# Optimization experiments

Measured on AMD Instinct MI355X. Metric: run time of the kernel, lower is better.

Reference implementation:

```python
import jax, jax.numpy as jnp
import numpy as np
from jax.scipy.linalg import solve_triangular
from jax.scipy.special import logsumexp

N, K, D = 131072, 32, 32
LOG_2PI = np.float32(np.log(2.0 * np.pi))


def setup_inputs() -> dict:
    key = jax.random.key(0)
    k1, k2, k3, k4 = jax.random.split(key, 4)
    X = jax.random.normal(k1, (N, D), dtype=jnp.float32)
    means = jax.random.normal(k2, (K, D), dtype=jnp.float32)
    chols = jax.random.normal(k3, (K, D, D), dtype=jnp.float32)
    weights = jax.random.normal(k4, (K,), dtype=jnp.float32) - 1.0  # normal_(-1, 1)
    return {"X": X, "means": means, "chols": chols, "weights": weights, "it": 0}


def _neglog_likelihood(X, means, chols, weights):
    d = X.shape[-1]
    n = X.shape[0]
    eye = jnp.eye(d, dtype=X.dtype)
    # sigmas[k] = chols[k] @ chols[k]^T + I  -> (K, D, D)
    sigmas = jnp.einsum('kij,klj->kil', chols, chols) + eye
    L = jnp.linalg.cholesky(sigmas)                      # (K, D, D)
    # per-cluster Gaussian log-densities for all points, batched
    diff = X[None, :, :] - means[:, None, :]             # (K, N, D)
    y = solve_triangular(L, diff.transpose(0, 2, 1), lower=True)  # (K, D, N)
    maha = jnp.sum(y * y, axis=1)                        # (K, N)
    logdet = 2.0 * jnp.sum(jnp.log(jnp.diagonal(L, axis1=-2, axis2=-1)), axis=-1)  # (K,)
    log_dens = -0.5 * (maha + (logdet + d * LOG_2PI)[:, None])    # (K, N)
    dens = jnp.exp(log_dens)                             # (K, N)
    # sum_{i,j} w_i w_j N_i(x) N_j(x) = (sum_k w_k N_k(x))^2
    numer = jnp.square(weights @ dens)                   # (N,)
    # pairwise normaliser Z_ij = N(mu_i; mu_j, S_i + S_j), all pairs batched
    S_ij = sigmas[:, None] + sigmas[None, :]             # (K, K, D, D)
    L_ij = jnp.linalg.cholesky(S_ij)
    dmu = means[:, None, :] - means[None, :, :]          # (K, K, D)
    y_ij = solve_triangular(L_ij, dmu[..., None], lower=True)[..., 0]  # (K, K, D)
    maha_ij = jnp.sum(y_ij * y_ij, axis=-1)              # (K, K)
    logdet_ij = 2.0 * jnp.sum(jnp.log(jnp.diagonal(L_ij, axis1=-2, axis2=-1)), axis=-1)
    Z_ij = jnp.exp(-0.5 * (maha_ij + logdet_ij + d * LOG_2PI))
    z = jnp.sum((weights[:, None] * weights[None, :]) * Z_ij)
    pdf = numer / z                                      # (N,)
    logp = jnp.log(pdf)                                  # (N,)
    return -(logsumexp(logp, axis=0) / n)


def reference(X, means, chols, weights, it):
    return _neglog_likelihood(X, means, chols, weights)
```

## Files before the change

### kernel.cpp

```cpp
#include <hip/hip_runtime.h>
#include <math.h>

#define NPTS  131072
#define NPTB  512
#define NPRB  256
#define GRID  (NPTB + NPRB)
#define DLOG2PIF 58.8120661f
#define DLOG2PI  58.81206612467475
#define SHIFT 92.0f
#define NEGHALF_LOG2E -0.72134752044f
#define LOG2E 1.44269504089f

typedef __attribute__((ext_vector_type(8)))  short short8;
typedef __attribute__((ext_vector_type(16))) float f32x16;

static __device__ __forceinline__ unsigned bfh(float f) {
  unsigned u = __float_as_uint(f);
  return (u + 0x7FFFu + ((u >> 16) & 1u)) >> 16;
}
static __device__ __forceinline__ float bfhf(float f) {
  return __uint_as_float(bfh(f) << 16);
}
static __device__ __forceinline__ short8 mk_a2(unsigned w) {
  int4 t = {(int)w, 0, 0, 0};
  return __builtin_bit_cast(short8, t);
}

__global__ __launch_bounds__(256) void setup_kernel(
    const float* __restrict__ means, const float* __restrict__ chols,
    const float* __restrict__ wts,
    uint4* __restrict__ Afrag, float* __restrict__ Kc, float* __restrict__ Sg,
    unsigned* __restrict__ ticket)
{
  const int tid = threadIdx.x, wv = tid >> 6, lane = tid & 63;
  const int r = lane & 31, h = lane >> 5;
  const int k = blockIdx.x*4 + wv;
  __shared__ float SshA[4][1056];
  __shared__ float blsA[4][1056];
  float* Ssh = SshA[wv];
  float* bls = blsA[wv];
  if (blockIdx.x == 0 && tid == 0) *ticket = 0u;
  const float* cp = chols + (size_t)k*1024 + r*32;
  float4 fa = *(const float4*)(cp + h*8);
  float4 fb = *(const float4*)(cp + h*8 + 4);
  float4 fc = *(const float4*)(cp + 16 + h*8);
  float4 fd = *(const float4*)(cp + 16 + h*8 + 4);
  float v0[8] = {fa.x,fa.y,fa.z,fa.w,fb.x,fb.y,fb.z,fb.w};
  float v1[8] = {fc.x,fc.y,fc.z,fc.w,fd.x,fd.y,fd.z,fd.w};
  short8 hi0, hi1, lo0, lo1;
  #pragma unroll
  for (int j = 0; j < 8; j++) {
    hi0[j] = (short)bfh(v0[j]);  lo0[j] = (short)bfh(v0[j] - bfhf(v0[j]));
    hi1[j] = (short)bfh(v1[j]);  lo1[j] = (short)bfh(v1[j] - bfhf(v1[j]));
  }
  f32x16 acc = {};
  acc = __builtin_amdgcn_mfma_f32_32x32x16_bf16(hi0, hi0, acc, 0,0,0);
  acc = __builtin_amdgcn_mfma_f32_32x32x16_bf16(hi1, hi1, acc, 0,0,0);
  acc = __builtin_amdgcn_mfma_f32_32x32x16_bf16(hi0, lo0, acc, 0,0,0);
  acc = __builtin_amdgcn_mfma_f32_32x32x16_bf16(hi1, lo1, acc, 0,0,0);
  acc = __builtin_amdgcn_mfma_f32_32x32x16_bf16(lo0, hi0, acc, 0,0,0);
  acc = __builtin_amdgcn_mfma_f32_32x32x16_bf16(lo1, hi1, acc, 0,0,0);
  #pragma unroll
  for (int q = 0; q < 16; q++) {
    int row = (q & 3) + 8*(q >> 2) + 4*h;
    Ssh[row*33 + r] = acc[q] + ((row == r) ? 1.0f : 0.0f);
  }
  float a[32];
  #pragma unroll
  for (int j = 0; j < 32; j++) a[j] = Ssh[r*33 + j];
  float ldsum = 0.0f;
  #pragma unroll
  for (int j = 0; j < 32; j++) {
    float dd = __shfl(a[j], j);
    float inv = __frsqrt_rn(dd);
    float sq = dd * inv;
    ldsum += __logf(sq);
    float l = a[j] * inv;
    #pragma unroll
    for (int e = j+1; e < 32; e++) {
      float le = __shfl(l, e);
      a[e] = (r >= e) ? fmaf(-l, le, a[e]) : a[e];
    }
    a[j] = (r == j) ? sq : ((r > j) ? l : a[j]);
  }
  #pragma unroll
  for (int j = 0; j < 32; j++) Ssh[r*33 + j] = a[j];
  #pragma unroll 1
  for (int d = 0; d < 32; d++) {
    float s0 = (d == r) ? 1.0f : 0.0f, s1 = 0.0f;
    int j = 0;
    for (; j + 1 < d; j += 2) {
      s0 = fmaf(-Ssh[d*33 + j],     bls[j*33 + r],     s0);
      s1 = fmaf(-Ssh[d*33 + j + 1], bls[(j+1)*33 + r], s1);
    }
    if (j < d) s0 = fmaf(-Ssh[d*33 + j], bls[j*33 + r], s0);
    bls[d*33 + r] = (s0 + s1) / Ssh[d*33 + d];
  }
  float t0[8], t1[8];
  #pragma unroll
  for (int j = 0; j < 8; j++) {
    t0[j] = bls[r*33 + h*8 + j];
    t1[j] = bls[r*33 + 16 + h*8 + j];
  }
  uint4 s0 = make_uint4(bfh(t0[0])|(bfh(t0[1])<<16), bfh(t0[2])|(bfh(t0[3])<<16),
                        bfh(t0[4])|(bfh(t0[5])<<16), bfh(t0[6])|(bfh(t0[7])<<16));
  uint4 s1 = make_uint4(bfh(t1[0])|(bfh(t1[1])<<16), bfh(t1[2])|(bfh(t1[3])<<16),
                        bfh(t1[4])|(bfh(t1[5])<<16), bfh(t1[6])|(bfh(t1[7])<<16));
  float cvp = 0.0f;
  #pragma unroll
  for (int j = 0; j < 8; j++) {
    cvp = fmaf(t0[j], means[k*32 + h*8 + j], cvp);
    cvp = fmaf(t1[j], means[k*32 + 16 + h*8 + j], cvp);
  }
  float cv = cvp + __shfl_xor(cvp, 32);
  unsigned ch = bfh(cv) ^ 0x8000u;
  unsigned cl = bfh(cv - bfhf(cv)) ^ 0x8000u;
  uint4 s2 = make_uint4((h == 0) ? (ch | (cl<<16)) : 0u, 0u, 0u, 0u);
  Afrag[(k*3 + 0)*64 + lane] = s0;
  Afrag[(k*3 + 1)*64 + lane] = s1;
  Afrag[(k*3 + 2)*64 + lane] = s2;
  if (lane == 0) {
    float wk = wts[k];
    float ld2 = 2.0f*ldsum + DLOG2PIF;
    Kc[k] = LOG2E*(SHIFT - 0.5f*ld2) + log2f(fabsf(wk));
    Sg[k] = (wk < 0.0f) ? -1.0f : 1.0f;
  }
}

__global__ __launch_bounds__(256) void work_kernel(
    const float* __restrict__ X, const float* __restrict__ means,
    const float* __restrict__ chols, const float* __restrict__ wts,
    const uint4* __restrict__ Afrag, const float* __restrict__ Kc,
    const float* __restrict__ Sg,
    double* __restrict__ zterm, double* __restrict__ partials,
    unsigned* __restrict__ ticket, float* __restrict__ out)
{
  __shared__ __align__(16) char smem[24576];
  __shared__ float K2sh[32], sksh[32];
  __shared__ double redd[4], redz[4];
  __shared__ unsigned lastFlag;
  const int tid = threadIdx.x, wv = tid >> 6, lane = tid & 63;
  const int r = lane & 31, h = lane >> 5;
  if (blockIdx.x < NPTB) {
    uint4* fsh = (uint4*)smem;
    const unsigned* fshw = (const unsigned*)smem;
    if (tid < 32) { K2sh[tid] = Kc[tid]; sksh[tid] = Sg[tid]; }
    const int n0 = blockIdx.x*256 + wv*64 + r;
    short8 xh00, xh01, xh10, xh11, x2c;
    {
      const float* xp0 = X + (size_t)n0*32;
      const float* xp1 = X + (size_t)(n0+32)*32;
      float4 fa = *(const float4*)(xp0 + h*8);
      float4 fb = *(const float4*)(xp0 + h*8 + 4);
      float4 fc = *(const float4*)(xp0 + 16 + h*8);
      float4 fd = *(const float4*)(xp0 + 16 + h*8 + 4);
      float4 ga = *(const float4*)(xp1 + h*8);
      float4 gb = *(const float4*)(xp1 + h*8 + 4);
      float4 gc = *(const float4*)(xp1 + 16 + h*8);
      float4 gd = *(const float4*)(xp1 + 16 + h*8 + 4);
      float v00[8] = {fa.x,fa.y,fa.z,fa.w,fb.x,fb.y,fb.z,fb.w};
      float v01[8] = {fc.x,fc.y,fc.z,fc.w,fd.x,fd.y,fd.z,fd.w};
      float v10[8] = {ga.x,ga.y,ga.z,ga.w,gb.x,gb.y,gb.z,gb.w};
      float v11[8] = {gc.x,gc.y,gc.z,gc.w,gd.x,gd.y,gd.z,gd.w};
      #pragma unroll
      for (int j = 0; j < 8; j++) {
        xh00[j] = (short)bfh(v00[j]);  xh01[j] = (short)bfh(v01[j]);
        xh10[j] = (short)bfh(v10[j]);  xh11[j] = (short)bfh(v11[j]);
        x2c[j] = 0;
      }
      if (h == 0) { x2c[0] = (short)0x3F80; x2c[1] = (short)0x3F80; }
    }
    float sF0 = 0.0f, sF1 = 0.0f;
    #pragma unroll 1
    for (int ph = 0; ph < 4; ph++) {
      __syncthreads();
      const uint4* src = Afrag + ph*1536;
      #pragma unroll
      for (int t = tid; t < 1536; t += 256) fsh[t] = src[t];
      __syncthreads();
      #pragma unroll 4
      for (int kk = 0; kk < 8; kk++) {
        const short8* fp = (const short8*)(fsh + kk*192);
        short8 a0 = fp[lane], a1 = fp[64+lane];
        short8 a2 = mk_a2(fshw[(kk*192 + 128 + lane)*4]);
        const int kidx = ph*8 + kk;
        const float Kk = K2sh[kidx], sk = sksh[kidx];
        f32x16 acc0 = {}, acc1 = {};
        acc0 = __builtin_amdgcn_mfma_f32_32x32x16_bf16(a0, xh00, acc0, 0,0,0);
        acc0 = __builtin_amdgcn_mfma_f32_32x32x16_bf16(a1, xh01, acc0, 0,0,0);
        acc0 = __builtin_amdgcn_mfma_f32_32x32x16_bf16(a2, x2c,  acc0, 0,0,0);
        acc1 = __builtin_amdgcn_mfma_f32_32x32x16_bf16(a0, xh10, acc1, 0,0,0);
        acc1 = __builtin_amdgcn_mfma_f32_32x32x16_bf16(a1, xh11, acc1, 0,0,0);
        acc1 = __builtin_amdgcn_mfma_f32_32x32x16_bf16(a2, x2c,  acc1, 0,0,0);
        float m0a=0.f, m0b=0.f, m1a=0.f, m1b=0.f;
        #pragma unroll
        for (int q = 0; q < 8; q++) {
          m0a = fmaf(acc0[q],   acc0[q],   m0a);
          m0b = fmaf(acc0[q+8], acc0[q+8], m0b);
          m1a = fmaf(acc1[q],   acc1[q],   m1a);
          m1b = fmaf(acc1[q+8], acc1[q+8], m1b);
        }
        float m0 = m0a + m0b, m1 = m1a + m1b;
        m0 += __shfl_xor(m0, 32);
        m1 += __shfl_xor(m1, 32);
        sF0 = fmaf(sk, exp2f(fmaf(m0, NEGHALF_LOG2E, Kk)), sF0);
        sF1 = fmaf(sk, exp2f(fmaf(m1, NEGHALF_LOG2E, Kk)), sF1);
      }
    }
    double Tp = (double)sF0*(double)sF0 + (double)sF1*(double)sF1;
    if (lane >= 32) Tp = 0.0;
    #pragma unroll
    for (int off = 32; off > 0; off >>= 1) Tp += __shfl_down(Tp, off);
    if (lane == 0) redd[wv] = Tp;
    __syncthreads();
    if (tid == 0) partials[blockIdx.x] = redd[0] + redd[1] + redd[2] + redd[3];
  } else {
    float* Ssh = (float*)smem + wv*1056;
    const int pid = (blockIdx.x - NPTB)*4 + wv, pi = pid >> 5, pj = pid & 31;
    const float* cpi = chols + (size_t)pi*1024 + r*32;
    const float* cpj = chols + (size_t)pj*1024 + r*32;
    float4 ia = *(const float4*)(cpi + h*8);
    float4 ib = *(const float4*)(cpi + h*8 + 4);
    float4 ic = *(const float4*)(cpi + 16 + h*8);
    float4 id = *(const float4*)(cpi + 16 + h*8 + 4);
    float4 ja = *(const float4*)(cpj + h*8);
    float4 jb = *(const float4*)(cpj + h*8 + 4);
    float4 jc = *(const float4*)(cpj + 16 + h*8);
    float4 jd = *(const float4*)(cpj + 16 + h*8 + 4);
    float vi0[8] = {ia.x,ia.y,ia.z,ia.w,ib.x,ib.y,ib.z,ib.w};
    float vi1[8] = {ic.x,ic.y,ic.z,ic.w,id.x,id.y,id.z,id.w};
    float vj0[8] = {ja.x,ja.y,ja.z,ja.w,jb.x,jb.y,jb.z,jb.w};
    float vj1[8] = {jc.x,jc.y,jc.z,jc.w,jd.x,jd.y,jd.z,jd.w};
    short8 I0h,I0l,I1h,I1l,J0h,J0l,J1h,J1l;
    #pragma unroll
    for (int j = 0; j < 8; j++) {
      I0h[j]=(short)bfh(vi0[j]); I0l[j]=(short)bfh(vi0[j]-bfhf(vi0[j]));
      I1h[j]=(short)bfh(vi1[j]); I1l[j]=(short)bfh(vi1[j]-bfhf(vi1[j]));
      J0h[j]=(short)bfh(vj0[j]); J0l[j]=(short)bfh(vj0[j]-bfhf(vj0[j]));
      J1h[j]=(short)bfh(vj1[j]); J1l[j]=(short)bfh(vj1[j]-bfhf(vj1[j]));
    }
    f32x16 pacc = {};
    pacc = __builtin_amdgcn_mfma_f32_32x32x16_bf16(I0h, I0h, pacc, 0,0,0);
    pacc = __builtin_amdgcn_mfma_f32_32x32x16_bf16(I1h, I1h, pacc, 0,0,0);
    pacc = __builtin_amdgcn_mfma_f32_32x32x16_bf16(I0h, I0l, pacc, 0,0,0);
    pacc = __builtin_amdgcn_mfma_f32_32x32x16_bf16(I1h, I1l, pacc, 0,0,0);
    pacc = __builtin_amdgcn_mfma_f32_32x32x16_bf16(I0l, I0h, pacc, 0,0,0);
    pacc = __builtin_amdgcn_mfma_f32_32x32x16_bf16(I1l, I1h, pacc, 0,0,0);
    pacc = __builtin_amdgcn_mfma_f32_32x32x16_bf16(J0h, J0h, pacc, 0,0,0);
    pacc = __builtin_amdgcn_mfma_f32_32x32x16_bf16(J1h, J1h, pacc, 0,0,0);
    pacc = __builtin_amdgcn_mfma_f32_32x32x16_bf16(J0h, J0l, pacc, 0,0,0);
    pacc = __builtin_amdgcn_mfma_f32_32x32x16_bf16(J1h, J1l, pacc, 0,0,0);
    pacc = __builtin_amdgcn_mfma_f32_32x32x16_bf16(J0l, J0h, pacc, 0,0,0);
    pacc = __builtin_amdgcn_mfma_f32_32x32x16_bf16(J1l, J1h, pacc, 0,0,0);
    #pragma unroll
    for (int q = 0; q < 16; q++) {
      int row = (q & 3) + 8*(q >> 2) + 4*h;
      Ssh[row*33 + r] = pacc[q] + ((row == r) ? 2.0f : 0.0f);
    }
    float a[32];
    #pragma unroll
    for (int j = 0; j < 32; j++) a[j] = Ssh[r*33 + j];
    #pragma unroll
    for (int j = 0; j < 32; j++) {
      float dd = __shfl(a[j], j);
      float inv = __frsqrt_rn(dd);
      float sq = dd * inv;
      float l = a[j] * inv;
      #pragma unroll
      for (int e = j+1; e < 32; e++) {
        float le = __shfl(l, e);
        a[e] = (r >= e) ? fmaf(-l, le, a[e]) : a[e];
      }
      a[j] = (r == j) ? sq : ((r > j) ? l : a[j]);
    }
    float acc2 = means[pi*32 + r] - means[pj*32 + r];
    float maha = 0.0f, ldsum = 0.0f;
    #pragma unroll
    for (int d = 0; d < 32; d++) {
      float dd = __shfl(a[d], d);
      float yd = __shfl(acc2, d) / dd;
      maha = fmaf(yd, yd, maha);
      ldsum += __logf(dd);
      acc2 = (r > d) ? fmaf(-a[d], yd, acc2) : acc2;
    }
    if (lane == 0) {
      double vd = -0.5 * ((double)maha + 2.0*(double)ldsum + DLOG2PI);
      zterm[pid] = (double)wts[pi] * (double)wts[pj] * exp(vd);
    }
  }
  __syncthreads();
  if (tid == 0) {
    __threadfence();
    lastFlag = (atomicAdd(ticket, 1u) == GRID - 1) ? 1u : 0u;
  }
  __syncthreads();
  if (lastFlag) {
    __threadfence();
    double t = 0.0, z = 0.0;
    for (int p = tid; p < NPTB; p += 256) t += partials[p];
    for (int p = tid; p < 1024; p += 256) z += zterm[p];
    #pragma unroll
    for (int off = 32; off > 0; off >>= 1) {
      t += __shfl_down(t, off);
      z += __shfl_down(z, off);
    }
    if (lane == 0) { redd[wv] = t; redz[wv] = z; }
    __syncthreads();
    if (tid == 0) {
      t = redd[0] + redd[1] + redd[2] + redd[3];
      z = redz[0] + redz[1] + redz[2] + redz[3];
      double logT = log(t) - 2.0*(double)SHIFT;
      double logz = log(z);
      out[0] = (float)((logz - logT) / (double)NPTS);
    }
  }
}

extern "C" void kernel_launch(void* const* d_in, const int* in_sizes, int n_in,
                              void* d_out, int out_size, void* d_ws, size_t ws_size,
                              hipStream_t stream) {
  const float* X     = (const float*)d_in[0];
  const float* means = (const float*)d_in[1];
  const float* chols = (const float*)d_in[2];
  const float* wts   = (const float*)d_in[3];
  float* out = (float*)d_out;
  char* ws = (char*)d_ws;
  uint4*    Afrag    = (uint4*)ws;
  float*    Kc       = (float*)(ws + 98304);
  float*    Sg       = (float*)(ws + 98432);
  double*   zterm    = (double*)(ws + 98560);
  double*   partials = (double*)(ws + 106752);
  unsigned* ticket   = (unsigned*)(ws + 110848);

  setup_kernel<<<8, 256, 0, stream>>>(means, chols, wts, Afrag, Kc, Sg, ticket);
  work_kernel<<<GRID, 256, 0, stream>>>(X, means, chols, wts, Afrag, Kc, Sg,
                                        zterm, partials, ticket, out);
}
```

Measured before the change: 129.5 us.

## Expand Mahalanobis distance algebraically to drop mean-offset MFMA and halve points per wave

```diff
diff --git a/kernel.cpp b/kernel.cpp
--- a/kernel.cpp
+++ b/kernel.cpp
@@ -2,7 +2,7 @@
 #include <math.h>
 
 #define NPTS  131072
-#define NPTB  512
+#define NPTB  1024
 #define NPRB  256
 #define GRID  (NPTB + NPRB)
 #define DLOG2PIF 58.8120661f
@@ -21,24 +21,19 @@
 static __device__ __forceinline__ float bfhf(float f) {
   return __uint_as_float(bfh(f) << 16);
 }
-static __device__ __forceinline__ short8 mk_a2(unsigned w) {
-  int4 t = {(int)w, 0, 0, 0};
-  return __builtin_bit_cast(short8, t);
-}
 
 __global__ __launch_bounds__(256) void setup_kernel(
     const float* __restrict__ means, const float* __restrict__ chols,
     const float* __restrict__ wts,
-    uint4* __restrict__ Afrag, float* __restrict__ Kc, float* __restrict__ Sg,
+    uint4* __restrict__ Afrag, float* __restrict__ gbuf,
+    float* __restrict__ Kc, float* __restrict__ Sg,
     unsigned* __restrict__ ticket)
 {
   const int tid = threadIdx.x, wv = tid >> 6, lane = tid & 63;
   const int r = lane & 31, h = lane >> 5;
   const int k = blockIdx.x*4 + wv;
   __shared__ float SshA[4][1056];
-  __shared__ float blsA[4][1056];
   float* Ssh = SshA[wv];
-  float* bls = blsA[wv];
   if (blockIdx.x == 0 && tid == 0) *ticket = 0u;
   const float* cp = chols + (size_t)k*1024 + r*32;
   float4 fa = *(const float4*)(cp + h*8);
@@ -72,7 +67,7 @@
   #pragma unroll
   for (int j = 0; j < 32; j++) {
     float dd = __shfl(a[j], j);
-    float inv = __frsqrt_rn(dd);
+    float inv = rsqrtf(dd);
     float sq = dd * inv;
     ldsum += __logf(sq);
     float l = a[j] * inv;
@@ -85,57 +80,61 @@
   }
   #pragma unroll
   for (int j = 0; j < 32; j++) Ssh[r*33 + j] = a[j];
-  #pragma unroll 1
+  float bv[32];
+  #pragma unroll
   for (int d = 0; d < 32; d++) {
     float s0 = (d == r) ? 1.0f : 0.0f, s1 = 0.0f;
-    int j = 0;
-    for (; j + 1 < d; j += 2) {
-      s0 = fmaf(-Ssh[d*33 + j],     bls[j*33 + r],     s0);
-      s1 = fmaf(-Ssh[d*33 + j + 1], bls[(j+1)*33 + r], s1);
-    }
-    if (j < d) s0 = fmaf(-Ssh[d*33 + j], bls[j*33 + r], s0);
-    bls[d*33 + r] = (s0 + s1) / Ssh[d*33 + d];
-  }
+    #pragma unroll
+    for (int j = 0; j + 1 < d; j += 2) {
+      s0 = fmaf(-Ssh[d*33 + j],     bv[j],   s0);
+      s1 = fmaf(-Ssh[d*33 + j + 1], bv[j+1], s1);
+    }
+    if (d & 1) s0 = fmaf(-Ssh[d*33 + (d-1)], bv[d-1], s0);
+    bv[d] = __fdividef(s0 + s1, Ssh[d*33 + d]);
+  }
+  #pragma unroll
+  for (int d = 0; d < 32; d++) Ssh[d*33 + r] = bv[d];
   float t0[8], t1[8];
   #pragma unroll
   for (int j = 0; j < 8; j++) {
-    t0[j] = bls[r*33 + h*8 + j];
-    t1[j] = bls[r*33 + 16 + h*8 + j];
+    t0[j] = Ssh[r*33 + h*8 + j];
+    t1[j] = Ssh[r*33 + 16 + h*8 + j];
   }
   uint4 s0 = make_uint4(bfh(t0[0])|(bfh(t0[1])<<16), bfh(t0[2])|(bfh(t0[3])<<16),
                         bfh(t0[4])|(bfh(t0[5])<<16), bfh(t0[6])|(bfh(t0[7])<<16));
   uint4 s1 = make_uint4(bfh(t1[0])|(bfh(t1[1])<<16), bfh(t1[2])|(bfh(t1[3])<<16),
                         bfh(t1[4])|(bfh(t1[5])<<16), bfh(t1[6])|(bfh(t1[7])<<16));
-  float cvp = 0.0f;
-  #pragma unroll
-  for (int j = 0; j < 8; j++) {
-    cvp = fmaf(t0[j], means[k*32 + h*8 + j], cvp);
-    cvp = fmaf(t1[j], means[k*32 + 16 + h*8 + j], cvp);
-  }
-  float cv = cvp + __shfl_xor(cvp, 32);
-  unsigned ch = bfh(cv) ^ 0x8000u;
-  unsigned cl = bfh(cv - bfhf(cv)) ^ 0x8000u;
-  uint4 s2 = make_uint4((h == 0) ? (ch | (cl<<16)) : 0u, 0u, 0u, 0u);
-  Afrag[(k*3 + 0)*64 + lane] = s0;
-  Afrag[(k*3 + 1)*64 + lane] = s1;
-  Afrag[(k*3 + 2)*64 + lane] = s2;
+  Afrag[(k*2 + 0)*64 + lane] = s0;
+  Afrag[(k*2 + 1)*64 + lane] = s1;
+  const float* mk = means + k*32;
+  float wr = 0.0f;
+  #pragma unroll
+  for (int j = 0; j < 32; j++) wr = fmaf(bfhf(Ssh[r*33 + j]), mk[j], wr);
+  float c = wr*wr;
+  #pragma unroll
+  for (int off = 16; off > 0; off >>= 1) c += __shfl_xor(c, off);
+  float gd = 0.0f;
+  #pragma unroll
+  for (int rr = 0; rr < 32; rr++)
+    gd = fmaf(bfhf(bv[rr]), __shfl(wr, rr), gd);
+  if (h == 0) gbuf[k*32 + r] = 2.0f*gd;
   if (lane == 0) {
     float wk = wts[k];
     float ld2 = 2.0f*ldsum + DLOG2PIF;
-    Kc[k] = LOG2E*(SHIFT - 0.5f*ld2) + log2f(fabsf(wk));
+    Kc[k] = LOG2E*(SHIFT - 0.5f*ld2 - 0.5f*c) + log2f(fabsf(wk));
     Sg[k] = (wk < 0.0f) ? -1.0f : 1.0f;
   }
 }
 
-__global__ __launch_bounds__(256) void work_kernel(
+__global__ __launch_bounds__(256, 4) void work_kernel(
     const float* __restrict__ X, const float* __restrict__ means,
     const float* __restrict__ chols, const float* __restrict__ wts,
-    const uint4* __restrict__ Afrag, const float* __restrict__ Kc,
-    const float* __restrict__ Sg,
+    const uint4* __restrict__ Afrag, const float* __restrict__ gbuf,
+    const float* __restrict__ Kc, const float* __restrict__ Sg,
     double* __restrict__ zterm, double* __restrict__ partials,
     unsigned* __restrict__ ticket, float* __restrict__ out)
 {
-  __shared__ __align__(16) char smem[24576];
+  __shared__ __align__(16) char smem[16896];
   __shared__ float K2sh[32], sksh[32];
   __shared__ double redd[4], redz[4];
   __shared__ unsigned lastFlag;
@@ -143,71 +142,79 @@
   const int r = lane & 31, h = lane >> 5;
   if (blockIdx.x < NPTB) {
     uint4* fsh = (uint4*)smem;
-    const unsigned* fshw = (const unsigned*)smem;
     if (tid < 32) { K2sh[tid] = Kc[tid]; sksh[tid] = Sg[tid]; }
-    const int n0 = blockIdx.x*256 + wv*64 + r;
-    short8 xh00, xh01, xh10, xh11, x2c;
+    const int n0 = blockIdx.x*128 + wv*32 + r;
+    short8 xh0, xh1;
     {
-      const float* xp0 = X + (size_t)n0*32;
-      const float* xp1 = X + (size_t)(n0+32)*32;
-      float4 fa = *(const float4*)(xp0 + h*8);
-      float4 fb = *(const float4*)(xp0 + h*8 + 4);
-      float4 fc = *(const float4*)(xp0 + 16 + h*8);
-      float4 fd = *(const float4*)(xp0 + 16 + h*8 + 4);
-      float4 ga = *(const float4*)(xp1 + h*8);
-      float4 gb = *(const float4*)(xp1 + h*8 + 4);
-      float4 gc = *(const float4*)(xp1 + 16 + h*8);
-      float4 gd = *(const float4*)(xp1 + 16 + h*8 + 4);
-      float v00[8] = {fa.x,fa.y,fa.z,fa.w,fb.x,fb.y,fb.z,fb.w};
-      float v01[8] = {fc.x,fc.y,fc.z,fc.w,fd.x,fd.y,fd.z,fd.w};
-      float v10[8] = {ga.x,ga.y,ga.z,ga.w,gb.x,gb.y,gb.z,gb.w};
-      float v11[8] = {gc.x,gc.y,gc.z,gc.w,gd.x,gd.y,gd.z,gd.w};
+      const float* xp = X + (size_t)n0*32;
+      float4 fa = *(const float4*)(xp + h*8);
+      float4 fb = *(const float4*)(xp + h*8 + 4);
+      float4 fc = *(const float4*)(xp + 16 + h*8);
+      float4 fd = *(const float4*)(xp + 16 + h*8 + 4);
+      float v0[8] = {fa.x,fa.y,fa.z,fa.w,fb.x,fb.y,fb.z,fb.w};
+      float v1[8] = {fc.x,fc.y,fc.z,fc.w,fd.x,fd.y,fd.z,fd.w};
+      #pragma unroll
+      for (int j = 0; j < 8; j++) { xh0[j] = (short)bfh(v0[j]); xh1[j] = (short)bfh(v1[j]); }
+    }
+    f32x16 accg = {};
+    {
+      const float* gp = gbuf + r*32 + h*8;
+      float4 ga = *(const float4*)(gp);
+      float4 gb = *(const float4*)(gp + 4);
+      float4 gc = *(const float4*)(gp + 16);
+      float4 gd = *(const float4*)(gp + 20);
+      float g0[8] = {ga.x,ga.y,ga.z,ga.w,gb.x,gb.y,gb.z,gb.w};
+      float g1[8] = {gc.x,gc.y,gc.z,gc.w,gd.x,gd.y,gd.z,gd.w};
+      short8 Gh0, Gl0, Gh1, Gl1;
       #pragma unroll
       for (int j = 0; j < 8; j++) {
-        xh00[j] = (short)bfh(v00[j]);  xh01[j] = (short)bfh(v01[j]);
-        xh10[j] = (short)bfh(v10[j]);  xh11[j] = (short)bfh(v11[j]);
-        x2c[j] = 0;
+        Gh0[j] = (short)bfh(g0[j]); Gl0[j] = (short)bfh(g0[j] - bfhf(g0[j]));
+        Gh1[j] = (short)bfh(g1[j]); Gl1[j] = (short)bfh(g1[j] - bfhf(g1[j]));
       }
-      if (h == 0) { x2c[0] = (short)0x3F80; x2c[1] = (short)0x3F80; }
-    }
-    float sF0 = 0.0f, sF1 = 0.0f;
-    #pragma unroll 1
+      accg = __builtin_amdgcn_mfma_f32_32x32x16_bf16(Gh0, xh0, accg, 0,0,0);
+      accg = __builtin_amdgcn_mfma_f32_32x32x16_bf16(Gl0, xh0, accg, 0,0,0);
+      accg = __builtin_amdgcn_mfma_f32_32x32x16_bf16(Gh1, xh1, accg, 0,0,0);
+      accg = __builtin_amdgcn_mfma_f32_32x32x16_bf16(Gl1, xh1, accg, 0,0,0);
+    }
+    float sF = 0.0f;
+    #pragma unroll
     for (int ph = 0; ph < 4; ph++) {
       __syncthreads();
-      const uint4* src = Afrag + ph*1536;
+      {
+        const uint4* src = Afrag + ph*1024;
+        uint4 t0 = src[tid], t1 = src[tid+256], t2 = src[tid+512], t3 = src[tid+768];
+        fsh[tid] = t0; fsh[tid+256] = t1; fsh[tid+512] = t2; fsh[tid+768] = t3;
+      }
+      __syncthreads();
+      const short8* cp0 = (const short8*)fsh;
+      short8 c0 = cp0[lane], c1 = cp0[64 + lane];
       #pragma unroll
-      for (int t = tid; t < 1536; t += 256) fsh[t] = src[t];
-      __syncthreads();
-      #pragma unroll 4
       for (int kk = 0; kk < 8; kk++) {
-        const short8* fp = (const short8*)(fsh + kk*192);
-        short8 a0 = fp[lane], a1 = fp[64+lane];
-        short8 a2 = mk_a2(fshw[(kk*192 + 128 + lane)*4]);
+        short8 nf0, nf1;
+        if (kk < 7) {
+          const short8* np = (const short8*)(fsh + (kk+1)*128);
+          nf0 = np[lane]; nf1 = np[64 + lane];
+        }
         const int kidx = ph*8 + kk;
         const float Kk = K2sh[kidx], sk = sksh[kidx];
-        f32x16 acc0 = {}, acc1 = {};
-        acc0 = __builtin_amdgcn_mfma_f32_32x32x16_bf16(a0, xh00, acc0, 0,0,0);
-        acc0 = __builtin_amdgcn_mfma_f32_32x32x16_bf16(a1, xh01, acc0, 0,0,0);
-        acc0 = __builtin_amdgcn_mfma_f32_32x32x16_bf16(a2, x2c,  acc0, 0,0,0);
-        acc1 = __builtin_amdgcn_mfma_f32_32x32x16_bf16(a0, xh10, acc1, 0,0,0);
-        acc1 = __builtin_amdgcn_mfma_f32_32x32x16_bf16(a1, xh11, acc1, 0,0,0);
-        acc1 = __builtin_amdgcn_mfma_f32_32x32x16_bf16(a2, x2c,  acc1, 0,0,0);
-        float m0a=0.f, m0b=0.f, m1a=0.f, m1b=0.f;
+        f32x16 acc2 = {};
+        acc2 = __builtin_amdgcn_mfma_f32_32x32x16_bf16(c0, xh0, acc2, 0,0,0);
+        acc2 = __builtin_amdgcn_mfma_f32_32x32x16_bf16(c1, xh1, acc2, 0,0,0);
+        float ma = 0.f, mb = 0.f;
         #pragma unroll
         for (int q = 0; q < 8; q++) {
-          m0a = fmaf(acc0[q],   acc0[q],   m0a);
-          m0b = fmaf(acc0[q+8], acc0[q+8], m0b);
-          m1a = fmaf(acc1[q],   acc1[q],   m1a);
-          m1b = fmaf(acc1[q+8], acc1[q+8], m1b);
+          ma = fmaf(acc2[q],   acc2[q],   ma);
+          mb = fmaf(acc2[q+8], acc2[q+8], mb);
         }
-        float m0 = m0a + m0b, m1 = m1a + m1b;
-        m0 += __shfl_xor(m0, 32);
-        m1 += __shfl_xor(m1, 32);
-        sF0 = fmaf(sk, exp2f(fmaf(m0, NEGHALF_LOG2E, Kk)), sF0);
-        sF1 = fmaf(sk, exp2f(fmaf(m1, NEGHALF_LOG2E, Kk)), sF1);
+        const int qg = (kidx & 3) | (((kidx >> 3) & 3) << 2);
+        const int hneed = (kidx >> 2) & 1;
+        float m = ma + mb - ((h == hneed) ? accg[qg] : 0.0f);
+        m += __shfl_xor(m, 32);
+        sF = fmaf(sk, exp2f(fmaf(m, NEGHALF_LOG2E, Kk)), sF);
+        c0 = nf0; c1 = nf1;
       }
     }
-    double Tp = (double)sF0*(double)sF0 + (double)sF1*(double)sF1;
+    double Tp = (double)sF*(double)sF;
     if (lane >= 32) Tp = 0.0;
     #pragma unroll
     for (int off = 32; off > 0; off >>= 1) Tp += __shfl_down(Tp, off);
@@ -326,13 +333,14 @@
   float* out = (float*)d_out;
   char* ws = (char*)d_ws;
   uint4*    Afrag    = (uint4*)ws;
-  float*    Kc       = (float*)(ws + 98304);
-  float*    Sg       = (float*)(ws + 98432);
-  double*   zterm    = (double*)(ws + 98560);
-  double*   partials = (double*)(ws + 106752);
-  unsigned* ticket   = (unsigned*)(ws + 110848);
-
-  setup_kernel<<<8, 256, 0, stream>>>(means, chols, wts, Afrag, Kc, Sg, ticket);
-  work_kernel<<<GRID, 256, 0, stream>>>(X, means, chols, wts, Afrag, Kc, Sg,
+  float*    gbuf     = (float*)(ws + 65536);
+  float*    Kc       = (float*)(ws + 69632);
+  float*    Sg       = (float*)(ws + 69760);
+  double*   zterm    = (double*)(ws + 69888);
+  double*   partials = (double*)(ws + 78080);
+  unsigned* ticket   = (unsigned*)(ws + 86272);
+
+  setup_kernel<<<8, 256, 0, stream>>>(means, chols, wts, Afrag, gbuf, Kc, Sg, ticket);
+  work_kernel<<<GRID, 256, 0, stream>>>(X, means, chols, wts, Afrag, gbuf, Kc, Sg,
                                         zterm, partials, ticket, out);
 }
```

Result: no change. 131.5 us (+1.5%).
